# Kernel tuning notes

Measured on AMD Instinct MI355X. Metric: run time of the kernel, lower is better.

Reference implementation:

```python
import jax, jax.numpy as jnp
import numpy as np
import math

EMBED_DIM = 1024
NUM_HEADS = 16
HEAD_DIM = EMBED_DIM // NUM_HEADS
D_FF = 4 * EMBED_DIM
EPS = 1e-6  # flax LayerNorm default


def _layer_norm(x, scale, bias):
    mu = jnp.mean(x, axis=-1, keepdims=True)
    var = jnp.mean(jnp.square(x - mu), axis=-1, keepdims=True)
    return (x - mu) * jax.lax.rsqrt(var + EPS) * scale + bias


def setup_inputs() -> dict:
    key = jax.random.key(0)
    ks = jax.random.split(key, 12)
    B, T, D = 8, 1024, EMBED_DIM
    x = jax.random.normal(ks[0], (B, T, D), dtype=jnp.float32)
    # causal mask broadcastable to [B, H, T, T]
    mask = jnp.tril(jnp.ones((T, T), dtype=bool))[None, None, :, :]
    mask = jnp.broadcast_to(mask, (B, 1, T, T))
    s = 0.02
    return {
        "x": x,
        "mask": mask,
        "ln1_scale": jnp.ones((D,), jnp.float32),
        "ln1_bias": jnp.zeros((D,), jnp.float32),
        "wq": jax.random.normal(ks[1], (D, D), jnp.float32) * s,
        "bq": jnp.zeros((D,), jnp.float32),
        "wk": jax.random.normal(ks[2], (D, D), jnp.float32) * s,
        "bk": jnp.zeros((D,), jnp.float32),
        "wv": jax.random.normal(ks[3], (D, D), jnp.float32) * s,
        "bv": jnp.zeros((D,), jnp.float32),
        "wo": jax.random.normal(ks[4], (D, D), jnp.float32) * s,
        "bo": jnp.zeros((D,), jnp.float32),
        "ln2_scale": jnp.ones((D,), jnp.float32),
        "ln2_bias": jnp.zeros((D,), jnp.float32),
        "w1": jax.random.normal(ks[5], (D, D_FF), jnp.float32) * s,
        "b1": jnp.zeros((D_FF,), jnp.float32),
        "w2": jax.random.normal(ks[6], (D_FF, D), jnp.float32) * s,
        "b2": jnp.zeros((D,), jnp.float32),
    }


def reference(x, mask, ln1_scale, ln1_bias, wq, bq, wk, bk, wv, bv, wo, bo,
              ln2_scale, ln2_bias, w1, b1, w2, b2):
    B, T, D = x.shape
    residual = x
    h = _layer_norm(x, ln1_scale, ln1_bias)
    q = (h @ wq + bq).reshape(B, T, NUM_HEADS, HEAD_DIM)
    k = (h @ wk + bk).reshape(B, T, NUM_HEADS, HEAD_DIM)
    v = (h @ wv + bv).reshape(B, T, NUM_HEADS, HEAD_DIM)
    # scores: [B, H, T, T]
    scores = jnp.einsum("bqhd,bkhd->bhqk", q, k) / math.sqrt(HEAD_DIM)
    scores = jnp.where(mask, scores, -1e9)
    probs = jax.nn.softmax(scores, axis=-1)
    # dropout is identity (deterministic=True)
    out = jnp.einsum("bhqk,bkhd->bqhd", probs, v).reshape(B, T, D)
    h = out @ wo + bo
    x = h + residual
    residual = x
    h = _layer_norm(x, ln2_scale, ln2_bias)
    h = jax.nn.gelu(h @ w1 + b1, approximate=True)  # flax nn.gelu default
    h = h @ w2 + b2
    return h + residual
```

## Files before the change

kernel.cpp:

```cpp
#include <hip/hip_runtime.h>
#include <hip/hip_bf16.h>

using bf16 = __hip_bfloat16;
typedef __attribute__((ext_vector_type(8))) short bf16x8;
typedef __attribute__((ext_vector_type(4))) float f32x4;

__device__ inline float u2f(unsigned int u) { return __uint_as_float(u << 16); }
__device__ inline float toF(float x) { return x; }
__device__ inline float toF(bf16 x) { return __bfloat162float(x); }
__device__ inline void storeO(float* p, float v) { *p = v; }
__device__ inline void storeO(bf16* p, float v) { *p = __float2bfloat16(v); }

__device__ inline void gload_lds16(const void* g, void* l) {
    __builtin_amdgcn_global_load_lds(
        (const __attribute__((address_space(1))) void*)g,
        (__attribute__((address_space(3))) void*)l, 16, 0, 0);
}

__device__ inline void wgbar() {
    asm volatile("s_waitcnt lgkmcnt(0)" ::: "memory");
    __builtin_amdgcn_s_barrier();
    asm volatile("" ::: "memory");
}

__device__ inline int swzb(int row, int bcol) {
    return row * 128 + (bcol ^ (((row ^ (row >> 3)) & 7) << 4));
}

__global__ __launch_bounds__(256) void transpose_k(const float* __restrict__ in,
                                                   bf16* __restrict__ out,
                                                   int R, int C) {
    __shared__ float tile[32][33];
    const int c0 = blockIdx.x * 32, r0 = blockIdx.y * 32;
    const int tx = threadIdx.x & 31, ty = threadIdx.x >> 5;
#pragma unroll
    for (int i = 0; i < 32; i += 8)
        tile[ty + i][tx] = in[(size_t)(r0 + ty + i) * C + (c0 + tx)];
    __syncthreads();
#pragma unroll
    for (int i = 0; i < 32; i += 8)
        out[(size_t)(c0 + ty + i) * R + (r0 + tx)] = __float2bfloat16(tile[tx][ty + i]);
}

__global__ __launch_bounds__(256) void catb_k(const float* __restrict__ a,
                                              const float* __restrict__ b,
                                              const float* __restrict__ c,
                                              float* __restrict__ o) {
    const int t = blockIdx.x * 256 + threadIdx.x;
    const float* s = t < 1024 ? a : (t < 2048 ? b : c);
    o[t] = s[t & 1023];
}

__device__ inline float waveRedSum(float x) {
#pragma unroll
    for (int off = 32; off; off >>= 1) x += __shfl_xor(x, off, 64);
    return x;
}

template <typename T>
__global__ __launch_bounds__(256) void layernorm_k(const T* __restrict__ in,
                                                   const float* __restrict__ g,
                                                   const float* __restrict__ bta,
                                                   bf16* __restrict__ out) {
    const int row = blockIdx.x, t = threadIdx.x;
    const int lane = t & 63, wid = t >> 6;
    const T* xr = in + (size_t)row * 1024;
    float v0, v1, v2, v3;
    if constexpr (sizeof(T) == 4) {
        float4 u = ((const float4*)xr)[t];
        v0 = u.x; v1 = u.y; v2 = u.z; v3 = u.w;
    } else {
        ushort4 u = ((const ushort4*)xr)[t];
        v0 = u2f(u.x); v1 = u2f(u.y); v2 = u2f(u.z); v3 = u2f(u.w);
    }
    __shared__ float red[8];
    float s = waveRedSum(v0 + v1 + v2 + v3);
    if (lane == 0) red[wid] = s;
    __syncthreads();
    float mu = (red[0] + red[1] + red[2] + red[3]) * (1.f / 1024.f);
    float d0 = v0 - mu, d1 = v1 - mu, d2 = v2 - mu, d3 = v3 - mu;
    float ss = waveRedSum(d0 * d0 + d1 * d1 + d2 * d2 + d3 * d3);
    if (lane == 0) red[4 + wid] = ss;
    __syncthreads();
    float var = (red[4] + red[5] + red[6] + red[7]) * (1.f / 1024.f);
    float inv = rsqrtf(var + 1e-6f);
    const int c = t * 4;
    bf16* orow = out + (size_t)row * 1024;
    orow[c + 0] = __float2bfloat16(d0 * inv * g[c + 0] + bta[c + 0]);
    orow[c + 1] = __float2bfloat16(d1 * inv * g[c + 1] + bta[c + 1]);
    orow[c + 2] = __float2bfloat16(d2 * inv * g[c + 2] + bta[c + 2]);
    orow[c + 3] = __float2bfloat16(d3 * inv * g[c + 3] + bta[c + 3]);
}

template <int GELU, int RES, int ACC, typename RT, typename OT>
__global__ __launch_bounds__(256) void mgemm_k(const bf16* __restrict__ A,
                                               const bf16* __restrict__ B, int ldB,
                                               const float* __restrict__ bias,
                                               const RT* __restrict__ resid,
                                               OT* C, int M, int N, int K) {
    __shared__ bf16 As[2 * 128 * 32];
    __shared__ bf16 Bs[2 * 128 * 32];
    const int tid = threadIdx.x;
    const int lane = tid & 63, wid = tid >> 6;
    const int l16 = lane & 15, quad = lane >> 4;
    const int wm = (wid >> 1) * 64, wn = (wid & 1) * 64;
    const int m0 = blockIdx.y * 128, n0 = blockIdx.x * 128;

    const int r0 = tid >> 2, sc0 = tid & 3;
    const int lc0 = sc0 ^ ((r0 >> 1) & 3);
    const int r1 = r0 + 64;
    const int lc1 = sc0 ^ ((r1 >> 1) & 3);
    const bf16* gA0 = A + (size_t)(m0 + r0) * K + lc0 * 8;
    const bf16* gA1 = A + (size_t)(m0 + r1) * K + lc1 * 8;
    const bf16* gB0 = B + (size_t)(n0 + r0) * ldB + lc0 * 8;
    const bf16* gB1 = B + (size_t)(n0 + r1) * ldB + lc1 * 8;
    char* asb = (char*)As;
    char* bsb = (char*)Bs;
    const int lb0 = wid * 1024, lb1 = 4096 + wid * 1024;
    const int rdsw = (quad ^ ((l16 >> 1) & 3)) * 16;

    f32x4 acc[4][4] = {};
    const int nT = K >> 5;
    gload_lds16(gA0, asb + lb0);
    gload_lds16(gA1, asb + lb1);
    gload_lds16(gB0, bsb + lb0);
    gload_lds16(gB1, bsb + lb1);
    __syncthreads();
    for (int t = 0; t < nT; ++t) {
        const int cur = t & 1;
        if (t + 1 < nT) {
            char* ab = asb + (cur ^ 1) * 8192;
            char* bb = bsb + (cur ^ 1) * 8192;
            const int ko = (t + 1) * 32;
            gload_lds16(gA0 + ko, ab + lb0);
            gload_lds16(gA1 + ko, ab + lb1);
            gload_lds16(gB0 + ko, bb + lb0);
            gload_lds16(gB1 + ko, bb + lb1);
        }
        const char* ar = asb + cur * 8192;
        const char* br = bsb + cur * 8192;
        bf16x8 a[4], b[4];
#pragma unroll
        for (int i = 0; i < 4; ++i)
            a[i] = *(const bf16x8*)(ar + (wm + i * 16 + l16) * 64 + rdsw);
#pragma unroll
        for (int i = 0; i < 4; ++i)
            b[i] = *(const bf16x8*)(br + (wn + i * 16 + l16) * 64 + rdsw);
#pragma unroll
        for (int mi = 0; mi < 4; ++mi)
#pragma unroll
            for (int ni = 0; ni < 4; ++ni)
                acc[mi][ni] = __builtin_amdgcn_mfma_f32_16x16x32_bf16(
                    a[mi], b[ni], acc[mi][ni], 0, 0, 0);
        __syncthreads();
    }
#pragma unroll
    for (int mi = 0; mi < 4; ++mi) {
#pragma unroll
        for (int ni = 0; ni < 4; ++ni) {
            const int col = n0 + wn + ni * 16 + l16;
            const float bv = bias ? bias[col] : 0.f;
#pragma unroll
            for (int r = 0; r < 4; ++r) {
                const int row = m0 + wm + mi * 16 + quad * 4 + r;
                float val = acc[mi][ni][r] + bv;
                if (GELU) {
                    float z = 0.7978845608028654f * (val + 0.044715f * val * val * val);
                    float th = 1.f - 2.f / (__expf(2.f * z) + 1.f);
                    val = 0.5f * val * (1.f + th);
                }
                const size_t idx = (size_t)row * N + col;
                if (RES) val += toF(resid[idx]);
                if (ACC) val += toF(C[idx]);
                storeO(&C[idx], val);
            }
        }
    }
}

__global__ __launch_bounds__(256) void attn_k(const bf16* __restrict__ q,
                                              const bf16* __restrict__ k,
                                              const bf16* __restrict__ v,
                                              bf16* __restrict__ o, int rs) {
    const int b = blockIdx.z, h = blockIdx.y;
    const int qi = 3 - blockIdx.x;
    const int qblock = qi * 256;
    const int tid = threadIdx.x;
    const int wave = tid >> 6, lane = tid & 63;
    const int l16 = lane & 15, quad = lane >> 4;
    const int q0w = qblock + wave * 64;

    __shared__ __align__(16) bf16 Kl[64 * 64];
    __shared__ __align__(16) bf16 Vt[64 * 64];
    __shared__ __align__(16) bf16 Pl[4 * 64 * 64];
    __shared__ __align__(16) float sc[4][64];

    bf16x8 qf[4][2];
#pragma unroll
    for (int ni = 0; ni < 4; ++ni) {
        const int row = q0w + ni * 16 + l16;
        const bf16* qp = q + ((size_t)b * 1024 + row) * rs + h * 64;
#pragma unroll
        for (int kc = 0; kc < 2; ++kc)
            qf[ni][kc] = *(const bf16x8*)(qp + kc * 32 + quad * 8);
    }

    f32x4 acc[4][4] = {};
    float mrun[4], lrun[4];
#pragma unroll
    for (int ni = 0; ni < 4; ++ni) { mrun[ni] = -1e30f; lrun[ni] = 0.f; }

    const int NT = qi * 4 + 4;
    const int myNT = qi * 4 + wave + 1;

    const int kr_ = tid >> 3, kch = tid & 7;
    const int vr_ = (tid >> 3) * 2, vdb = (tid & 7) * 8;
    uint4 kA, kB, vA, vB;
    {
        const size_t gk = ((size_t)b * 1024 + 0 + kr_) * rs + h * 64 + kch * 8;
        kA = *(const uint4*)(k + gk);
        kB = *(const uint4*)(k + gk + (size_t)32 * rs);
        const size_t gv = ((size_t)b * 1024 + 0 + vr_) * rs + h * 64 + vdb;
        vA = *(const uint4*)(v + gv);
        vB = *(const uint4*)(v + gv + rs);
    }

    for (int t = 0; t < NT; ++t) {
        wgbar();
        *(uint4*)((char*)Kl + swzb(kr_, kch * 16)) = kA;
        *(uint4*)((char*)Kl + swzb(kr_ + 32, kch * 16)) = kB;
        {
            const unsigned aw[4] = {vA.x, vA.y, vA.z, vA.w};
            const unsigned bw[4] = {vB.x, vB.y, vB.z, vB.w};
#pragma unroll
            for (int j = 0; j < 8; ++j) {
                const unsigned lo = (aw[j >> 1] >> ((j & 1) * 16)) & 0xffffu;
                const unsigned hi = (bw[j >> 1] >> ((j & 1) * 16)) & 0xffffu;
                *(unsigned*)((char*)Vt + swzb(vdb + j, vr_ * 2)) = lo | (hi << 16);
            }
        }
        if (t + 1 < NT) {
            const int j1 = (t + 1) * 64;
            const size_t gk = ((size_t)b * 1024 + j1 + kr_) * rs + h * 64 + kch * 8;
            kA = *(const uint4*)(k + gk);
            kB = *(const uint4*)(k + gk + (size_t)32 * rs);
            const size_t gv = ((size_t)b * 1024 + j1 + vr_) * rs + h * 64 + vdb;
            vA = *(const uint4*)(v + gv);
            vB = *(const uint4*)(v + gv + rs);
        }
        wgbar();
        if (t < myNT) {
            const int j0 = t * 64;
            f32x4 st[4][4] = {};
#pragma unroll
            for (int kc = 0; kc < 2; ++kc) {
                bf16x8 kf[4];
#pragma unroll
                for (int mi = 0; mi < 4; ++mi)
                    kf[mi] = *(const bf16x8*)((char*)Kl +
                             swzb(mi * 16 + l16, kc * 64 + quad * 16));
#pragma unroll
                for (int mi = 0; mi < 4; ++mi)
#pragma unroll
                    for (int ni = 0; ni < 4; ++ni)
                        st[mi][ni] = __builtin_amdgcn_mfma_f32_16x16x32_bf16(
                            kf[mi], qf[ni][kc], st[mi][ni], 0, 0, 0);
            }
            if (j0 == q0w) {
#pragma unroll
                for (int mi = 0; mi < 4; ++mi)
#pragma unroll
                    for (int ni = 0; ni < 4; ++ni)
#pragma unroll
                        for (int r = 0; r < 4; ++r)
                            if (mi * 16 + quad * 4 + r > ni * 16 + l16)
                                st[mi][ni][r] = -1e30f;
            }
            float fac[4];
#pragma unroll
            for (int ni = 0; ni < 4; ++ni) {
                float mx = -1e30f;
#pragma unroll
                for (int mi = 0; mi < 4; ++mi)
#pragma unroll
                    for (int r = 0; r < 4; ++r) mx = fmaxf(mx, st[mi][ni][r]);
                mx = fmaxf(mx, __shfl_xor(mx, 16, 64));
                mx = fmaxf(mx, __shfl_xor(mx, 32, 64));
                const float nm = fmaxf(mrun[ni], mx);
                fac[ni] = __expf((mrun[ni] - nm) * 0.125f);
                mrun[ni] = nm;
                float ls = 0.f;
#pragma unroll
                for (int mi = 0; mi < 4; ++mi)
#pragma unroll
                    for (int r = 0; r < 4; ++r) {
                        const float p = __expf((st[mi][ni][r] - nm) * 0.125f);
                        st[mi][ni][r] = p;
                        ls += p;
                    }
                ls += __shfl_xor(ls, 16, 64);
                ls += __shfl_xor(ls, 32, 64);
                lrun[ni] = lrun[ni] * fac[ni] + ls;
            }
            if (quad == 0)
#pragma unroll
                for (int ni = 0; ni < 4; ++ni) sc[wave][ni * 16 + l16] = fac[ni];
#pragma unroll
            for (int mi = 0; mi < 4; ++mi) {
                const f32x4 f4 = *(const f32x4*)&sc[wave][mi * 16 + quad * 4];
#pragma unroll
                for (int ni = 0; ni < 4; ++ni)
#pragma unroll
                    for (int r = 0; r < 4; ++r) acc[mi][ni][r] *= f4[r];
            }
            char* Pb = (char*)Pl + wave * 8192;
#pragma unroll
            for (int ni = 0; ni < 4; ++ni) {
                const int qrow = ni * 16 + l16;
#pragma unroll
                for (int mi = 0; mi < 4; ++mi) {
                    union { bf16 bv[4]; uint2 u2; } pk;
#pragma unroll
                    for (int r = 0; r < 4; ++r)
                        pk.bv[r] = __float2bfloat16(st[mi][ni][r]);
                    *(uint2*)(Pb + swzb(qrow, mi * 32 + quad * 8)) = pk.u2;
                }
            }
#pragma unroll
            for (int kc = 0; kc < 2; ++kc) {
                bf16x8 pf[4], vf[4];
#pragma unroll
                for (int mi = 0; mi < 4; ++mi)
                    pf[mi] = *(const bf16x8*)(Pb +
                             swzb(mi * 16 + l16, kc * 64 + quad * 16));
#pragma unroll
                for (int ni = 0; ni < 4; ++ni)
                    vf[ni] = *(const bf16x8*)((char*)Vt +
                             swzb(ni * 16 + l16, kc * 64 + quad * 16));
#pragma unroll
                for (int mi = 0; mi < 4; ++mi)
#pragma unroll
                    for (int ni = 0; ni < 4; ++ni)
                        acc[mi][ni] = __builtin_amdgcn_mfma_f32_16x16x32_bf16(
                            pf[mi], vf[ni], acc[mi][ni], 0, 0, 0);
            }
        }
    }
    if (quad == 0)
#pragma unroll
        for (int ni = 0; ni < 4; ++ni) sc[wave][ni * 16 + l16] = lrun[ni];
#pragma unroll
    for (int mi = 0; mi < 4; ++mi) {
        const f32x4 l4 = *(const f32x4*)&sc[wave][mi * 16 + quad * 4];
#pragma unroll
        for (int r = 0; r < 4; ++r) {
            const float inv = 1.f / l4[r];
            const int row = q0w + mi * 16 + quad * 4 + r;
            bf16* orow = o + ((size_t)b * 1024 + row) * 1024 + h * 64;
#pragma unroll
            for (int ni = 0; ni < 4; ++ni)
                orow[ni * 16 + l16] = __float2bfloat16(acc[mi][ni][r] * inv);
        }
    }
}

extern "C" void kernel_launch(void* const* d_in, const int* in_sizes, int n_in,
                              void* d_out, int out_size, void* d_ws, size_t ws_size,
                              hipStream_t stream) {
    (void)out_size; (void)ws_size;
    const float* x = (const float*)d_in[0];
    const int base = (n_in >= 18 && in_sizes[1] > 4096) ? 2 : 1;
    const float* ln1s = (const float*)d_in[base + 0];
    const float* ln1b = (const float*)d_in[base + 1];
    const float* wq   = (const float*)d_in[base + 2];
    const float* bq   = (const float*)d_in[base + 3];
    const float* wk   = (const float*)d_in[base + 4];
    const float* bk   = (const float*)d_in[base + 5];
    const float* wv   = (const float*)d_in[base + 6];
    const float* bv   = (const float*)d_in[base + 7];
    const float* wo   = (const float*)d_in[base + 8];
    const float* bo   = (const float*)d_in[base + 9];
    const float* ln2s = (const float*)d_in[base + 10];
    const float* ln2b = (const float*)d_in[base + 11];
    const float* w1   = (const float*)d_in[base + 12];
    const float* b1   = (const float*)d_in[base + 13];
    const float* w2   = (const float*)d_in[base + 14];
    const float* b2   = (const float*)d_in[base + 15];
    float* out = (float*)d_out;

    char* ws = (char*)d_ws;
    char* oc = (char*)d_out;
    const size_t MB = 1ull << 20;
    bf16* h     = (bf16*)(ws + 0 * MB);
    bf16* qkv   = (bf16*)(ws + 16 * MB);
    bf16* ao    = (bf16*)(ws + 0 * MB);
    bf16* h2    = (bf16*)(ws + 0 * MB);
    bf16* woT   = (bf16*)(ws + 16 * MB);
    bf16* f1c   = (bf16*)(ws + 16 * MB);
    bf16* w1T   = (bf16*)(ws + 48 * MB);
    bf16* w2T   = (bf16*)(ws + 56 * MB);
    bf16* wqkvT = (bf16*)(oc + 0 * MB);
    float* bqkv = (float*)(oc + 8 * MB);

    const dim3 tb(256);

    layernorm_k<float><<<8192, tb, 0, stream>>>(x, ln1s, ln1b, h);
    transpose_k<<<dim3(32, 32), tb, 0, stream>>>(wq, wqkvT, 1024, 1024);
    transpose_k<<<dim3(32, 32), tb, 0, stream>>>(wk, wqkvT + 1024 * 1024, 1024, 1024);
    transpose_k<<<dim3(32, 32), tb, 0, stream>>>(wv, wqkvT + 2 * 1024 * 1024, 1024, 1024);
    catb_k<<<12, tb, 0, stream>>>(bq, bk, bv, bqkv);
    mgemm_k<0, 0, 0, float, bf16><<<dim3(24, 64), tb, 0, stream>>>(
        h, wqkvT, 1024, bqkv, nullptr, qkv, 8192, 3072, 1024);
    attn_k<<<dim3(4, 16, 8), tb, 0, stream>>>(qkv, qkv + 1024, qkv + 2048, ao, 3072);
    transpose_k<<<dim3(32, 32), tb, 0, stream>>>(wo, woT, 1024, 1024);
    transpose_k<<<dim3(128, 32), tb, 0, stream>>>(w1, w1T, 1024, 4096);
    transpose_k<<<dim3(32, 128), tb, 0, stream>>>(w2, w2T, 4096, 1024);
    mgemm_k<0, 1, 0, float, float><<<dim3(8, 64), tb, 0, stream>>>(
        ao, woT, 1024, bo, x, out, 8192, 1024, 1024);
    layernorm_k<float><<<8192, tb, 0, stream>>>(out, ln2s, ln2b, h2);
    for (int c = 0; c < 2; ++c) {
        mgemm_k<1, 0, 0, float, bf16><<<dim3(16, 64), tb, 0, stream>>>(
            h2, w1T + (size_t)c * 2048 * 1024, 1024, b1 + c * 2048, nullptr,
            f1c, 8192, 2048, 1024);
        mgemm_k<0, 0, 1, float, float><<<dim3(8, 64), tb, 0, stream>>>(
            f1c, w2T + c * 2048, 4096, c ? nullptr : b2, nullptr,
            out, 8192, 1024, 2048);
    }
}
```

Baseline: 642.0 us.

## Remap GEMM/attention workgroups across XCDs, add MFMA priority, lazy softmax rescale

The GEMM grid is flattened and each block index is remapped so that consecutive tiles land on the same XCD (blockIdx mod 8), aiming for better L2 reuse on the chiplet design. The attention grid is flattened too and interleaves causal q-blocks of opposite cost across batches to balance the load. MFMA loops are wrapped in s_setprio to favour matrix issue. Online softmax now rescales the accumulator only when the new max exceeds the running max by a threshold, which skips the exp and LDS round trip on most tiles. The cost is a threshold that could let exponentials grow large.

```diff
diff --git a/kernel.cpp b/kernel.cpp
--- a/kernel.cpp
+++ b/kernel.cpp
@@ -97,14 +97,16 @@
                                                const bf16* __restrict__ B, int ldB,
                                                const float* __restrict__ bias,
                                                const RT* __restrict__ resid,
-                                               OT* C, int M, int N, int K) {
+                                               OT* C, int M, int N, int K, int gx) {
     __shared__ bf16 As[2 * 128 * 32];
     __shared__ bf16 Bs[2 * 128 * 32];
     const int tid = threadIdx.x;
     const int lane = tid & 63, wid = tid >> 6;
     const int l16 = lane & 15, quad = lane >> 4;
     const int wm = (wid >> 1) * 64, wn = (wid & 1) * 64;
-    const int m0 = blockIdx.y * 128, n0 = blockIdx.x * 128;
+    const int nwg = gridDim.x;
+    const int wg = ((blockIdx.x & 7) * (nwg >> 3)) + (blockIdx.x >> 3);
+    const int m0 = (wg / gx) * 128, n0 = (wg % gx) * 128;
 
     const int r0 = tid >> 2, sc0 = tid & 3;
     const int lc0 = sc0 ^ ((r0 >> 1) & 3);
@@ -146,12 +148,14 @@
 #pragma unroll
         for (int i = 0; i < 4; ++i)
             b[i] = *(const bf16x8*)(br + (wn + i * 16 + l16) * 64 + rdsw);
+        __builtin_amdgcn_s_setprio(1);
 #pragma unroll
         for (int mi = 0; mi < 4; ++mi)
 #pragma unroll
             for (int ni = 0; ni < 4; ++ni)
                 acc[mi][ni] = __builtin_amdgcn_mfma_f32_16x16x32_bf16(
                     a[mi], b[ni], acc[mi][ni], 0, 0, 0);
+        __builtin_amdgcn_s_setprio(0);
         __syncthreads();
     }
 #pragma unroll
@@ -182,8 +186,12 @@
                                               const bf16* __restrict__ k,
                                               const bf16* __restrict__ v,
                                               bf16* __restrict__ o, int rs) {
-    const int b = blockIdx.z, h = blockIdx.y;
-    const int qi = 3 - blockIdx.x;
+    const int bid = blockIdx.x;
+    const int u = bid & 255, top = bid >> 8;
+    const int xx = u & 3;
+    const int h = (u >> 2) & 15;
+    const int b = top * 4 + (u >> 6);
+    const int qi = top ? 3 - xx : xx;
     const int qblock = qi * 256;
     const int tid = threadIdx.x;
     const int wave = tid >> 6, lane = tid & 63;
@@ -259,12 +267,14 @@
                 for (int mi = 0; mi < 4; ++mi)
                     kf[mi] = *(const bf16x8*)((char*)Kl +
                              swzb(mi * 16 + l16, kc * 64 + quad * 16));
+                __builtin_amdgcn_s_setprio(1);
 #pragma unroll
                 for (int mi = 0; mi < 4; ++mi)
 #pragma unroll
                     for (int ni = 0; ni < 4; ++ni)
                         st[mi][ni] = __builtin_amdgcn_mfma_f32_16x16x32_bf16(
                             kf[mi], qf[ni][kc], st[mi][ni], 0, 0, 0);
+                __builtin_amdgcn_s_setprio(0);
             }
             if (j0 == q0w) {
 #pragma unroll
@@ -276,42 +286,64 @@
                             if (mi * 16 + quad * 4 + r > ni * 16 + l16)
                                 st[mi][ni][r] = -1e30f;
             }
-            float fac[4];
+            float mx[4];
 #pragma unroll
             for (int ni = 0; ni < 4; ++ni) {
-                float mx = -1e30f;
-#pragma unroll
-                for (int mi = 0; mi < 4; ++mi)
-#pragma unroll
-                    for (int r = 0; r < 4; ++r) mx = fmaxf(mx, st[mi][ni][r]);
-                mx = fmaxf(mx, __shfl_xor(mx, 16, 64));
-                mx = fmaxf(mx, __shfl_xor(mx, 32, 64));
-                const float nm = fmaxf(mrun[ni], mx);
-                fac[ni] = __expf((mrun[ni] - nm) * 0.125f);
-                mrun[ni] = nm;
-                float ls = 0.f;
-#pragma unroll
-                for (int mi = 0; mi < 4; ++mi)
-#pragma unroll
-                    for (int r = 0; r < 4; ++r) {
-                        const float p = __expf((st[mi][ni][r] - nm) * 0.125f);
-                        st[mi][ni][r] = p;
-                        ls += p;
-                    }
+                float a0 = fmaxf(st[0][ni][0], st[0][ni][1]);
+                float a1 = fmaxf(st[0][ni][2], st[0][ni][3]);
+                float a2 = fmaxf(st[1][ni][0], st[1][ni][1]);
+                float a3 = fmaxf(st[1][ni][2], st[1][ni][3]);
+                float a4 = fmaxf(st[2][ni][0], st[2][ni][1]);
+                float a5 = fmaxf(st[2][ni][2], st[2][ni][3]);
+                float a6 = fmaxf(st[3][ni][0], st[3][ni][1]);
+                float a7 = fmaxf(st[3][ni][2], st[3][ni][3]);
+                float m_ = fmaxf(fmaxf(fmaxf(a0, a1), fmaxf(a2, a3)),
+                                 fmaxf(fmaxf(a4, a5), fmaxf(a6, a7)));
+                m_ = fmaxf(m_, __shfl_xor(m_, 16, 64));
+                m_ = fmaxf(m_, __shfl_xor(m_, 32, 64));
+                mx[ni] = m_;
+            }
+            const bool need = (mx[0] > mrun[0] + 64.f) | (mx[1] > mrun[1] + 64.f) |
+                              (mx[2] > mrun[2] + 64.f) | (mx[3] > mrun[3] + 64.f);
+            if (__any(need)) {
+                float fac[4];
+#pragma unroll
+                for (int ni = 0; ni < 4; ++ni) {
+                    const float nm = (mx[ni] > mrun[ni] + 64.f) ? mx[ni] : mrun[ni];
+                    fac[ni] = __expf((mrun[ni] - nm) * 0.125f);
+                    mrun[ni] = nm;
+                    lrun[ni] *= fac[ni];
+                }
+                if (quad == 0)
+#pragma unroll
+                    for (int ni = 0; ni < 4; ++ni) sc[wave][ni * 16 + l16] = fac[ni];
+#pragma unroll
+                for (int mi = 0; mi < 4; ++mi) {
+                    const f32x4 f4 = *(const f32x4*)&sc[wave][mi * 16 + quad * 4];
+#pragma unroll
+                    for (int ni = 0; ni < 4; ++ni)
+#pragma unroll
+                        for (int r = 0; r < 4; ++r) acc[mi][ni][r] *= f4[r];
+                }
+            }
+#pragma unroll
+            for (int ni = 0; ni < 4; ++ni) {
+                const float mm = mrun[ni];
+                float t0 = 0.f, t1 = 0.f, t2 = 0.f, t3 = 0.f;
+#pragma unroll
+                for (int mi = 0; mi < 4; ++mi) {
+                    float p0 = __expf((st[mi][ni][0] - mm) * 0.125f);
+                    float p1 = __expf((st[mi][ni][1] - mm) * 0.125f);
+                    float p2 = __expf((st[mi][ni][2] - mm) * 0.125f);
+                    float p3 = __expf((st[mi][ni][3] - mm) * 0.125f);
+                    st[mi][ni][0] = p0; st[mi][ni][1] = p1;
+                    st[mi][ni][2] = p2; st[mi][ni][3] = p3;
+                    t0 += p0; t1 += p1; t2 += p2; t3 += p3;
+                }
+                float ls = (t0 + t1) + (t2 + t3);
                 ls += __shfl_xor(ls, 16, 64);
                 ls += __shfl_xor(ls, 32, 64);
-                lrun[ni] = lrun[ni] * fac[ni] + ls;
-            }
-            if (quad == 0)
-#pragma unroll
-                for (int ni = 0; ni < 4; ++ni) sc[wave][ni * 16 + l16] = fac[ni];
-#pragma unroll
-            for (int mi = 0; mi < 4; ++mi) {
-                const f32x4 f4 = *(const f32x4*)&sc[wave][mi * 16 + quad * 4];
-#pragma unroll
-                for (int ni = 0; ni < 4; ++ni)
-#pragma unroll
-                    for (int r = 0; r < 4; ++r) acc[mi][ni][r] *= f4[r];
+                lrun[ni] += ls;
             }
             char* Pb = (char*)Pl + wave * 8192;
 #pragma unroll
@@ -337,12 +369,14 @@
                 for (int ni = 0; ni < 4; ++ni)
                     vf[ni] = *(const bf16x8*)((char*)Vt +
                              swzb(ni * 16 + l16, kc * 64 + quad * 16));
+                __builtin_amdgcn_s_setprio(1);
 #pragma unroll
                 for (int mi = 0; mi < 4; ++mi)
 #pragma unroll
                     for (int ni = 0; ni < 4; ++ni)
                         acc[mi][ni] = __builtin_amdgcn_mfma_f32_16x16x32_bf16(
                             pf[mi], vf[ni], acc[mi][ni], 0, 0, 0);
+                __builtin_amdgcn_s_setprio(0);
             }
         }
     }
@@ -409,21 +443,21 @@
     transpose_k<<<dim3(32, 32), tb, 0, stream>>>(wk, wqkvT + 1024 * 1024, 1024, 1024);
     transpose_k<<<dim3(32, 32), tb, 0, stream>>>(wv, wqkvT + 2 * 1024 * 1024, 1024, 1024);
     catb_k<<<12, tb, 0, stream>>>(bq, bk, bv, bqkv);
-    mgemm_k<0, 0, 0, float, bf16><<<dim3(24, 64), tb, 0, stream>>>(
-        h, wqkvT, 1024, bqkv, nullptr, qkv, 8192, 3072, 1024);
-    attn_k<<<dim3(4, 16, 8), tb, 0, stream>>>(qkv, qkv + 1024, qkv + 2048, ao, 3072);
+    mgemm_k<0, 0, 0, float, bf16><<<1536, tb, 0, stream>>>(
+        h, wqkvT, 1024, bqkv, nullptr, qkv, 8192, 3072, 1024, 24);
+    attn_k<<<512, tb, 0, stream>>>(qkv, qkv + 1024, qkv + 2048, ao, 3072);
     transpose_k<<<dim3(32, 32), tb, 0, stream>>>(wo, woT, 1024, 1024);
     transpose_k<<<dim3(128, 32), tb, 0, stream>>>(w1, w1T, 1024, 4096);
     transpose_k<<<dim3(32, 128), tb, 0, stream>>>(w2, w2T, 4096, 1024);
-    mgemm_k<0, 1, 0, float, float><<<dim3(8, 64), tb, 0, stream>>>(
-        ao, woT, 1024, bo, x, out, 8192, 1024, 1024);
+    mgemm_k<0, 1, 0, float, float><<<512, tb, 0, stream>>>(
+        ao, woT, 1024, bo, x, out, 8192, 1024, 1024, 8);
     layernorm_k<float><<<8192, tb, 0, stream>>>(out, ln2s, ln2b, h2);
     for (int c = 0; c < 2; ++c) {
-        mgemm_k<1, 0, 0, float, bf16><<<dim3(16, 64), tb, 0, stream>>>(
+        mgemm_k<1, 0, 0, float, bf16><<<1024, tb, 0, stream>>>(
             h2, w1T + (size_t)c * 2048 * 1024, 1024, b1 + c * 2048, nullptr,
-            f1c, 8192, 2048, 1024);
-        mgemm_k<0, 0, 1, float, float><<<dim3(8, 64), tb, 0, stream>>>(
+            f1c, 8192, 2048, 1024, 16);
+        mgemm_k<0, 0, 1, float, float><<<512, tb, 0, stream>>>(
             f1c, w2T + c * 2048, 4096, c ? nullptr : b2, nullptr,
-            out, 8192, 1024, 2048);
-    }
-}
+            out, 8192, 1024, 2048, 8);
+    }
+}
```

Result: faster. 584.3 us (-9.0%).
